# Kernel tuning notes

Measured on AMD Instinct MI355X. Metric: run time of the kernel, lower is better.

## Reference

```python
import jax, jax.numpy as jnp
import numpy as np
import math

B, N, D, H, K = 32, 512, 768, 12, 8  # batch, patches, hidden_dim, heads, n_topic_groups
HD = D // H


def setup_inputs() -> dict:
    key = jax.random.key(0)
    ks = jax.random.split(key, 12)
    hidden_states = jax.random.normal(ks[0], (B, N, D), jnp.float32)
    # group ids in 1..K, every group present (required by original sorted-dict indexing)
    tid = jax.random.permutation(ks[1], (jnp.arange(B, dtype=jnp.int64) % K) + 1)
    s = 1.0 / math.sqrt(D)
    def lin(k):
        kw, kb = jax.random.split(k)
        return (jax.random.normal(kw, (D, D), jnp.float32) * s,
                jax.random.normal(kb, (D,), jnp.float32) * s)
    Wq, bq = lin(ks[2])
    Wk, bk = lin(ks[3])
    Wv, bv = lin(ks[4])
    Wo, bo = lin(ks[5])
    Wc, bc = lin(ks[6])  # Conv1d(D, D, kernel_size=1) == pointwise linear
    return dict(hidden_states=hidden_states, tid=tid, Wq=Wq, bq=bq, Wk=Wk, bk=bk,
                Wv=Wv, bv=bv, Wo=Wo, bo=bo, Wc=Wc, bc=bc)


def reference(hidden_states, tid, Wq, bq, Wk, bk, Wv, bv, Wo, bo, Wc, bc):
    # --- context(): per-group context_aware + mean, scattered back ---
    # context_aware(x) = mean over group of (x + conv1x1(x)); conv is pointwise so
    # it commutes with grouping -> compute per-sample then segment-mean.
    y = hidden_states + jnp.einsum('bnd,ed->bne', hidden_states, Wc) + bc  # [B,N,D]
    seg = tid - 1  # ids are 1..K
    sums = jax.ops.segment_sum(y, seg, num_segments=K)                      # [K,N,D]
    counts = jax.ops.segment_sum(jnp.ones((B,), y.dtype), seg, num_segments=K)
    means = sums / jnp.maximum(counts, 1.0)[:, None, None]
    contexts = means[seg] + hidden_states                                   # [B,N,D]

    # --- dual-stage attention (dropout rate 0 / eval mode) ---
    def heads(x):  # [B,N,D] -> [B,H,N,HD]
        return x.reshape(B, N, H, HD).transpose(0, 2, 1, 3)

    q = heads(hidden_states @ Wq.T + bq)
    t = heads(contexts @ Wq.T + bq)  # topic_states also passes through self.query
    k = heads(hidden_states @ Wk.T + bk)
    v = heads(hidden_states @ Wv.T + bv)

    scale = 1.0 / math.sqrt(HD)
    p1 = jax.nn.softmax(jnp.einsum('bhqd,bhkd->bhqk', t, k) * scale, axis=-1)
    v_t = jnp.einsum('bhqk,bhkd->bhqd', p1, v)
    p2 = jax.nn.softmax(jnp.einsum('bhqd,bhkd->bhqk', q, t) * scale, axis=-1)
    ctx = jnp.einsum('bhqk,bhkd->bhqd', p2, v_t)

    ctx = ctx.transpose(0, 2, 1, 3).reshape(B, N, D)
    return ctx @ Wo.T + bo
```

## Files before the change

kernel.cpp:

```cpp
#include <hip/hip_runtime.h>
#include <hip/hip_bf16.h>


typedef __bf16 bf16_t;
typedef __bf16 bf16x8 __attribute__((ext_vector_type(8)));
typedef __bf16 bf16x4 __attribute__((ext_vector_type(4)));
typedef float f32x4 __attribute__((ext_vector_type(4)));

#define B_ 32
#define N_ 512
#define D_ 768
#define H_ 12
#define HD_ 64
#define K_ 8
#define ND_ (N_ * D_)

typedef __attribute__((address_space(1))) unsigned int as1_u32;
typedef __attribute__((address_space(3))) unsigned int as3_u32;

__device__ __forceinline__ void glds16(const void* g, void* l) {
  __builtin_amdgcn_global_load_lds((as1_u32*)g, (as3_u32*)l, 16, 0, 0);
}

__device__ __forceinline__ f32x4 mfma16(bf16x8 a, bf16x8 b, f32x4 c) {
  return __builtin_amdgcn_mfma_f32_16x16x32_bf16(a, b, c, 0, 0, 0);
}

__device__ __forceinline__ bf16x8 addv8(bf16x8 a, bf16x8 b) {
  bf16x8 o;
#pragma unroll
  for (int j = 0; j < 8; ++j) o[j] = (bf16_t)((float)a[j] + (float)b[j]);
  return o;
}

__device__ __forceinline__ int seg_of(const int* tid, int b) {
  const bool is64 = (tid[1] == 0);
  int v = is64 ? (int)((const long long*)tid)[b] : tid[b];
  return v - 1;
}

__device__ __forceinline__ void gemm_core(const bf16_t* __restrict__ A,
                                          const bf16_t* __restrict__ Bw,
                                          char* smem, f32x4 (&acc)[4][4]) {
  const int t = threadIdx.x;
  const int lane = t & 63, w = t >> 6;
  const int quad = lane >> 4, l15 = lane & 15;
  const int r0 = t >> 2;
  const int c0e = (t & 3) * 8;
  const int wbase = w * 1024;
  const int mRow = (w >> 1) * 64, nCol = (w & 1) * 64;

  const bf16_t* ga0 = A + (size_t)r0 * D_ + c0e;
  const bf16_t* ga1 = A + (size_t)(r0 + 64) * D_ + c0e;
  const bf16_t* gb0 = Bw + (size_t)r0 * D_ + c0e;
  const bf16_t* gb1 = Bw + (size_t)(r0 + 64) * D_ + c0e;

  glds16(ga0, smem + wbase);
  glds16(ga1, smem + 4096 + wbase);
  glds16(gb0, smem + 8192 + wbase);
  glds16(gb1, smem + 12288 + wbase);

  for (int kb = 0; kb < 24; ++kb) {
    __syncthreads();
    char* cur = smem + (kb & 1) * 16384;
    char* nxt = smem + ((kb + 1) & 1) * 16384;
    if (kb < 23) {
      const int ko = (kb + 1) * 32;
      glds16(ga0 + ko, nxt + wbase);
      glds16(ga1 + ko, nxt + 4096 + wbase);
      glds16(gb0 + ko, nxt + 8192 + wbase);
      glds16(gb1 + ko, nxt + 12288 + wbase);
    }
    bf16x8 af[4], bfr[4];
#pragma unroll
    for (int mt = 0; mt < 4; ++mt)
      af[mt] = *(const bf16x8*)(cur + (mRow + mt * 16 + l15) * 64 + quad * 16);
#pragma unroll
    for (int nt = 0; nt < 4; ++nt)
      bfr[nt] = *(const bf16x8*)(cur + 8192 + (nCol + nt * 16 + l15) * 64 +
                                 quad * 16);
#pragma unroll
    for (int mt = 0; mt < 4; ++mt)
#pragma unroll
      for (int nt = 0; nt < 4; ++nt)
        acc[mt][nt] = mfma16(af[mt], bfr[nt], acc[mt][nt]);
  }
}

__device__ __forceinline__ void zero_acc(f32x4 (&acc)[4][4]) {
  const f32x4 z = {0.f, 0.f, 0.f, 0.f};
#pragma unroll
  for (int a = 0; a < 4; ++a)
#pragma unroll
    for (int b = 0; b < 4; ++b) acc[a][b] = z;
}

__global__ __launch_bounds__(256) void k_front(
    const float* __restrict__ x, const float* __restrict__ Wq,
    const float* __restrict__ Wk, const float* __restrict__ Wv,
    const float* __restrict__ Wc, const float* __restrict__ Wo,
    const int* __restrict__ tid, bf16_t* __restrict__ Xb,
    bf16_t* __restrict__ Wqb, bf16_t* __restrict__ Wkb,
    bf16_t* __restrict__ Wvb, bf16_t* __restrict__ Wcb,
    bf16_t* __restrict__ Wob, bf16_t* __restrict__ Mx) {
  if (blockIdx.x < 192) {
    const size_t i = ((size_t)blockIdx.x * 256 + threadIdx.x) * 8;
    float acc[K_][8];
    float cntk[K_];
#pragma unroll
    for (int k = 0; k < K_; ++k) {
      cntk[k] = 0.f;
#pragma unroll
      for (int j = 0; j < 8; ++j) acc[k][j] = 0.f;
    }
    const bool is64 = (tid[1] == 0);
    for (int b = 0; b < B_; ++b) {
      const int s = (is64 ? (int)((const long long*)tid)[b] : tid[b]) - 1;
      const float* p = x + (size_t)b * ND_ + i;
      f32x4 y0 = *(const f32x4*)p;
      f32x4 y1 = *(const f32x4*)(p + 4);
      bf16x8 xo;
#pragma unroll
      for (int j = 0; j < 4; ++j) {
        xo[j] = (bf16_t)y0[j];
        xo[4 + j] = (bf16_t)y1[j];
      }
      *(bf16x8*)(Xb + (size_t)b * ND_ + i) = xo;
#pragma unroll
      for (int k = 0; k < K_; ++k) {
        const float msk = (s == k) ? 1.f : 0.f;
        cntk[k] += msk;
#pragma unroll
        for (int j = 0; j < 4; ++j) {
          acc[k][j] += msk * y0[j];
          acc[k][4 + j] += msk * y1[j];
        }
      }
    }
#pragma unroll
    for (int k = 0; k < K_; ++k) {
      const float inv = 1.f / fmaxf(cntk[k], 1.f);
      bf16x8 o;
#pragma unroll
      for (int j = 0; j < 8; ++j) o[j] = (bf16_t)(acc[k][j] * inv);
      *(bf16x8*)(Mx + (size_t)k * ND_ + i) = o;
    }
    return;
  }
  int bid = blockIdx.x - 192;
  const int wi = bid / 288;
  bid = bid % 288;
  const float* in = wi == 0 ? Wq : wi == 1 ? Wk : wi == 2 ? Wv : wi == 3 ? Wc
                                                                         : Wo;
  bf16_t* out = wi == 0 ? Wqb : wi == 1 ? Wkb : wi == 2 ? Wvb : wi == 3 ? Wcb
                                                                        : Wob;
  const size_t i = ((size_t)bid * 256 + threadIdx.x) * 8;
  f32x4 a = *(const f32x4*)(in + i);
  f32x4 b = *(const f32x4*)(in + i + 4);
  bf16x8 o;
#pragma unroll
  for (int j = 0; j < 4; ++j) { o[j] = (bf16_t)a[j]; o[4 + j] = (bf16_t)b[j]; }
  *(bf16x8*)(out + i) = o;
}

__global__ __launch_bounds__(256, 4) void k_mid(
    const bf16_t* __restrict__ X, const bf16_t* __restrict__ Wq,
    const bf16_t* __restrict__ Wk, const bf16_t* __restrict__ Wv,
    const float* __restrict__ bq, const float* __restrict__ bk,
    const float* __restrict__ bv, bf16_t* __restrict__ Q,
    bf16_t* __restrict__ Kb, bf16_t* __restrict__ V,
    const bf16_t* __restrict__ Mx, const bf16_t* __restrict__ Wcb,
    const float* __restrict__ bc, bf16_t* __restrict__ Mb) {
  __shared__ alignas(16) char smem[32768];
  const int lane = threadIdx.x & 63, w = threadIdx.x >> 6;
  const int quad = lane >> 4, l15 = lane & 15;

  if (blockIdx.x < 192) {
    const int mblk = blockIdx.x / 6, nblk = blockIdx.x % 6;
    f32x4 acc[4][4];
    zero_acc(acc);
    gemm_core(Mx + (size_t)mblk * 128 * D_, Wcb + (size_t)nblk * 128 * D_,
              smem, acc);
    const int mbase = mblk * 128 + (w >> 1) * 64;
    const int nbase = nblk * 128 + (w & 1) * 64;
#pragma unroll
    for (int nt = 0; nt < 4; ++nt) {
      const int col = nbase + nt * 16 + l15;
      const float bb = bc[col];
#pragma unroll
      for (int mt = 0; mt < 4; ++mt)
#pragma unroll
        for (int r = 0; r < 4; ++r) {
          const int row = mbase + mt * 16 + quad * 4 + r;
          const size_t oi = (size_t)row * D_ + col;
          Mb[oi] = (bf16_t)(acc[mt][nt][r] + bb + (float)Mx[oi]);
        }
    }
    return;
  }

  const int qbid = blockIdx.x - 192;
  const int xcd = qbid & 7, i = qbid >> 3;
  const int tile = i % 18, rowblk = (i / 18) * 8 + xcd;
  const int wsel = tile / 6, nb = tile % 6;
  const bf16_t* W = wsel == 0 ? Wq : wsel == 1 ? Wk : Wv;
  const float* bias = wsel == 0 ? bq : wsel == 1 ? bk : bv;
  bf16_t* Out = wsel == 0 ? Q : wsel == 1 ? Kb : V;

  f32x4 acc[4][4];
  zero_acc(acc);
  gemm_core(X + (size_t)rowblk * 128 * D_, W + (size_t)nb * 128 * D_, smem,
            acc);

  const int mbase = rowblk * 128 + (w >> 1) * 64;
  const int nbase = nb * 128 + (w & 1) * 64;
#pragma unroll
  for (int nt = 0; nt < 4; ++nt) {
    const int col = nbase + nt * 16 + l15;
    const float bb = bias[col];
#pragma unroll
    for (int mt = 0; mt < 4; ++mt)
#pragma unroll
      for (int r = 0; r < 4; ++r) {
        const int row = mbase + mt * 16 + quad * 4 + r;
        Out[(size_t)row * D_ + col] = (bf16_t)(acc[mt][nt][r] + bb);
      }
  }
}

__global__ __launch_bounds__(256) void k_gemm_plain(
    const bf16_t* __restrict__ A, const bf16_t* __restrict__ W,
    const float* __restrict__ bias, const bf16_t* __restrict__ addA,
    void* __restrict__ Out, int outF32, int swz) {
  __shared__ alignas(16) char smem[32768];
  int mblk, nblk;
  if (swz) {
    const int bid = blockIdx.x;
    const int xcd = bid & 7, i = bid >> 3;
    nblk = i % 6;
    mblk = (i / 6) * 8 + xcd;
  } else {
    mblk = blockIdx.x;
    nblk = blockIdx.y;
  }
  f32x4 acc[4][4];
  zero_acc(acc);
  gemm_core(A + (size_t)mblk * 128 * D_, W + (size_t)nblk * 128 * D_, smem,
            acc);
  const int lane = threadIdx.x & 63, w = threadIdx.x >> 6;
  const int quad = lane >> 4, l15 = lane & 15;
  const int mbase = mblk * 128 + (w >> 1) * 64;
  const int nbase = nblk * 128 + (w & 1) * 64;
#pragma unroll
  for (int nt = 0; nt < 4; ++nt) {
    const int col = nbase + nt * 16 + l15;
    const float bb = bias ? bias[col] : 0.f;
#pragma unroll
    for (int mt = 0; mt < 4; ++mt)
#pragma unroll
      for (int r = 0; r < 4; ++r) {
        const int row = mbase + mt * 16 + quad * 4 + r;
        float v = acc[mt][nt][r] + bb;
        if (addA) v += (float)addA[(size_t)row * D_ + col];
        const size_t oi = (size_t)row * D_ + col;
        if (outF32) ((float*)Out)[oi] = v;
        else ((bf16_t*)Out)[oi] = (bf16_t)v;
      }
  }
}

__global__ __launch_bounds__(256) void k_attn(const bf16_t* __restrict__ Qp,
                                              const bf16_t* __restrict__ Kp,
                                              const bf16_t* __restrict__ Vp,
                                              const bf16_t* __restrict__ Madd,
                                              const int* __restrict__ tid,
                                              bf16_t* __restrict__ Op,
                                              int addq) {
  __shared__ alignas(16) __bf16 Kt[64][72];
  __shared__ alignas(16) __bf16 Vt[64][72];
  __shared__ alignas(16) __bf16 Pl[4][32][72];

  const int lane = threadIdx.x & 63, w = threadIdx.x >> 6;
  const int quad = lane >> 4, l15 = lane & 15;
  const int b = blockIdx.y / H_, h = blockIdx.y % H_;
  const int q0 = blockIdx.x * 128 + w * 32;
  const size_t base = (size_t)b * ND_ + h * HD_;
  const float C = 0.18033688011112042f;
  const int sg = seg_of(tid, b);
  const bf16_t* Mh = Madd + (size_t)sg * ND_ + h * HD_;

  bf16x8 aq[2][2];
#pragma unroll
  for (int mt = 0; mt < 2; ++mt)
#pragma unroll
    for (int ks = 0; ks < 2; ++ks) {
      const size_t off = (size_t)(q0 + mt * 16 + l15) * D_ + ks * 32 + quad * 8;
      bf16x8 q = *(const bf16x8*)(Qp + base + off);
      if (addq == 1) q = addv8(q, *(const bf16x8*)(Mh + off));
      aq[mt][ks] = q;
    }

  f32x4 O[2][4];
  float lacc[2][4];
  {
    const f32x4 z = {0.f, 0.f, 0.f, 0.f};
#pragma unroll
    for (int mt = 0; mt < 2; ++mt)
#pragma unroll
      for (int nt = 0; nt < 4; ++nt) O[mt][nt] = z;
#pragma unroll
    for (int mt = 0; mt < 2; ++mt)
#pragma unroll
      for (int r = 0; r < 4; ++r) lacc[mt][r] = 0.f;
  }

  const int sr = threadIdx.x >> 2, sc = threadIdx.x & 3;
  const int sig_sr = ((sr & 15) << 2) | (sr >> 4);

  bf16x8 kr[2], vr[2];
#pragma unroll
  for (int half = 0; half < 2; ++half) {
    const int cc = sc + half * 4;
    const size_t off = (size_t)sr * D_ + cc * 8;
    bf16x8 kv = *(const bf16x8*)(Kp + base + off);
    if (addq == 2) kv = addv8(kv, *(const bf16x8*)(Mh + off));
    kr[half] = kv;
    vr[half] = *(const bf16x8*)(Vp + base + off);
  }

  for (int c0 = 0; c0 < N_; c0 += 64) {
    __syncthreads();
#pragma unroll
    for (int half = 0; half < 2; ++half) {
      const int cc = sc + half * 4;
      *(bf16x8*)(&Kt[sr][cc * 8]) = kr[half];
#pragma unroll
      for (int j = 0; j < 8; ++j) Vt[cc * 8 + j][sig_sr] = vr[half][j];
    }
    __syncthreads();

    if (c0 + 64 < N_) {
#pragma unroll
      for (int half = 0; half < 2; ++half) {
        const int cc = sc + half * 4;
        const size_t off = (size_t)(c0 + 64 + sr) * D_ + cc * 8;
        bf16x8 kv = *(const bf16x8*)(Kp + base + off);
        if (addq == 2) kv = addv8(kv, *(const bf16x8*)(Mh + off));
        kr[half] = kv;
        vr[half] = *(const bf16x8*)(Vp + base + off);
      }
    }

    f32x4 S[2][4];
    {
      const f32x4 z = {0.f, 0.f, 0.f, 0.f};
#pragma unroll
      for (int mt = 0; mt < 2; ++mt)
#pragma unroll
        for (int nt = 0; nt < 4; ++nt) S[mt][nt] = z;
    }
#pragma unroll
    for (int ks = 0; ks < 2; ++ks) {
      bf16x8 bk[4];
#pragma unroll
      for (int nt = 0; nt < 4; ++nt)
        bk[nt] = *(const bf16x8*)(&Kt[nt * 16 + l15][ks * 32 + quad * 8]);
#pragma unroll
      for (int mt = 0; mt < 2; ++mt)
#pragma unroll
        for (int nt = 0; nt < 4; ++nt)
          S[mt][nt] = mfma16(aq[mt][ks], bk[nt], S[mt][nt]);
    }

#pragma unroll
    for (int mt = 0; mt < 2; ++mt)
#pragma unroll
      for (int r = 0; r < 4; ++r) {
        bf16x4 pk;
#pragma unroll
        for (int nt = 0; nt < 4; ++nt) {
          const float p = exp2f(S[mt][nt][r] * C);
          lacc[mt][r] += p;
          pk[nt] = (bf16_t)p;
        }
        *(bf16x4*)(&Pl[w][mt * 16 + quad * 4 + r][l15 * 4]) = pk;
      }

#pragma unroll
    for (int ks2 = 0; ks2 < 2; ++ks2) {
      bf16x8 ap[2], bv[4];
#pragma unroll
      for (int mt = 0; mt < 2; ++mt)
        ap[mt] = *(const bf16x8*)(&Pl[w][mt * 16 + l15][ks2 * 32 + quad * 8]);
#pragma unroll
      for (int nt2 = 0; nt2 < 4; ++nt2)
        bv[nt2] = *(const bf16x8*)(&Vt[nt2 * 16 + l15][ks2 * 32 + quad * 8]);
#pragma unroll
      for (int mt = 0; mt < 2; ++mt)
#pragma unroll
        for (int nt2 = 0; nt2 < 4; ++nt2)
          O[mt][nt2] = mfma16(ap[mt], bv[nt2], O[mt][nt2]);
    }
  }

#pragma unroll
  for (int mt = 0; mt < 2; ++mt)
#pragma unroll
    for (int r = 0; r < 4; ++r) {
      float l = lacc[mt][r];
#pragma unroll
      for (int d = 1; d < 16; d <<= 1) l += __shfl_xor(l, d);
      const float inv = 1.f / l;
      const size_t row = base + (size_t)(q0 + mt * 16 + quad * 4 + r) * D_;
#pragma unroll
      for (int nt2 = 0; nt2 < 4; ++nt2)
        Op[row + nt2 * 16 + l15] = (bf16_t)(O[mt][nt2][r] * inv);
    }
}

__global__ __launch_bounds__(256) void k_zero(float* __restrict__ out) {
  const size_t i = ((size_t)blockIdx.x * 256 + threadIdx.x) * 8;
  f32x4 z = {0.f, 0.f, 0.f, 0.f};
  *(f32x4*)(out + i) = z;
  *(f32x4*)(out + i + 4) = z;
}

extern "C" void kernel_launch(void* const* d_in, const int* in_sizes, int n_in,
                              void* d_out, int out_size, void* d_ws,
                              size_t ws_size, hipStream_t stream) {
  const float* x  = (const float*)d_in[0];
  const int*  tid = (const int*)d_in[1];
  const float* Wq = (const float*)d_in[2];
  const float* bq = (const float*)d_in[3];
  const float* Wk = (const float*)d_in[4];
  const float* bk = (const float*)d_in[5];
  const float* Wv = (const float*)d_in[6];
  const float* bv = (const float*)d_in[7];
  const float* Wo = (const float*)d_in[8];
  const float* bo = (const float*)d_in[9];
  const float* Wc = (const float*)d_in[10];
  const float* bc = (const float*)d_in[11];

  const size_t SZ  = (size_t)B_ * ND_ * sizeof(bf16_t);
  const size_t MSZ = (size_t)K_ * ND_ * sizeof(bf16_t);
  const size_t WSZ = (size_t)D_ * D_ * sizeof(bf16_t);
  if (ws_size < 3 * SZ + MSZ + 5 * WSZ) {
    k_zero<<<6144, 256, 0, stream>>>((float*)d_out);
    return;
  }

  char* ws = (char*)d_ws;
  bf16_t* Qb  = (bf16_t*)(ws);
  bf16_t* Kb  = (bf16_t*)(ws + SZ);
  bf16_t* Vb  = (bf16_t*)(ws + 2 * SZ);
  bf16_t* Mq  = (bf16_t*)(ws + 3 * SZ);
  bf16_t* Wqb = (bf16_t*)(ws + 3 * SZ + MSZ);
  bf16_t* Wkb = (bf16_t*)(ws + 3 * SZ + MSZ + WSZ);
  bf16_t* Wvb = (bf16_t*)(ws + 3 * SZ + MSZ + 2 * WSZ);
  bf16_t* Wcb = (bf16_t*)(ws + 3 * SZ + MSZ + 3 * WSZ);
  bf16_t* Wob = (bf16_t*)(ws + 3 * SZ + MSZ + 4 * WSZ);
  bf16_t* Mx  = Mq;
  bf16_t* Mb  = (bf16_t*)d_out;
  bf16_t* VT  = (bf16_t*)d_out;
  bf16_t* Xb  = (bf16_t*)d_out + (size_t)B_ * ND_;
  bf16_t* CTX = Kb;

  k_front<<<1632, 256, 0, stream>>>(x, Wq, Wk, Wv, Wc, Wo, tid, Xb, Wqb, Wkb,
                                    Wvb, Wcb, Wob, Mx);
  k_mid<<<2496, 256, 0, stream>>>(Xb, Wqb, Wkb, Wvb, bq, bk, bv, Qb, Kb, Vb,
                                  Mx, Wcb, bc, Mb);
  k_gemm_plain<<<dim3(32, 6), 256, 0, stream>>>(Mb, Wqb, nullptr, nullptr, Mq,
                                                0, 0);
  k_attn<<<dim3(4, B_ * H_), 256, 0, stream>>>(Qb, Kb, Vb, Mq, tid, VT, 1);
  k_attn<<<dim3(4, B_ * H_), 256, 0, stream>>>(Qb, Qb, VT, Mq, tid, CTX, 2);
  k_gemm_plain<<<768, 256, 0, stream>>>(CTX, Wob, bo, nullptr, d_out, 1, 1);
}
```

Baseline: 397.2 us.

## Fold conv1x1 weight into query projection to drop a GEMM pass

Precomputes a combined weight Wq·(I+Wc) and bias Wq·bc in the front kernel, so the group-mean topic queries come from one GEMM on the group means instead of a conv GEMM followed by a separate query GEMM. This removes one kernel launch and the intermediate Mb round trip. In exchange the front kernel gains a small fp32-input weight GEMM and a bias matvec, and the rounding changes because the folded weight is stored in bf16.

```diff
diff --git a/kernel.cpp b/kernel.cpp
--- a/kernel.cpp
+++ b/kernel.cpp
@@ -99,12 +99,108 @@
     const float* __restrict__ x, const float* __restrict__ Wq,
     const float* __restrict__ Wk, const float* __restrict__ Wv,
     const float* __restrict__ Wc, const float* __restrict__ Wo,
-    const int* __restrict__ tid, bf16_t* __restrict__ Xb,
-    bf16_t* __restrict__ Wqb, bf16_t* __restrict__ Wkb,
-    bf16_t* __restrict__ Wvb, bf16_t* __restrict__ Wcb,
-    bf16_t* __restrict__ Wob, bf16_t* __restrict__ Mx) {
-  if (blockIdx.x < 192) {
-    const size_t i = ((size_t)blockIdx.x * 256 + threadIdx.x) * 8;
+    const float* __restrict__ bc, const int* __restrict__ tid,
+    bf16_t* __restrict__ Xb, bf16_t* __restrict__ Wqb,
+    bf16_t* __restrict__ Wkb, bf16_t* __restrict__ Wvb,
+    bf16_t* __restrict__ Wcb, bf16_t* __restrict__ Wob,
+    bf16_t* __restrict__ Mx, bf16_t* __restrict__ Wqcb,
+    float* __restrict__ bq2) {
+  __shared__ alignas(16) char smem[16384];
+  const int t = threadIdx.x;
+
+  if (blockIdx.x < 36) {
+    const int mblk = blockIdx.x / 6, nblk = blockIdx.x % 6;
+    const int lane = t & 63, w = t >> 6;
+    const int quad = lane >> 4, l15 = lane & 15;
+    const int mRow = (w >> 1) * 64, nCol = (w & 1) * 64;
+    const int ar = t >> 2, ac = (t & 3) * 8;
+    const int bd = t >> 3, bc0 = (t & 7) * 16;
+    const float* gA0 = Wq + (size_t)(mblk * 128 + ar) * D_ + ac;
+    const float* gA1 = gA0 + (size_t)64 * D_;
+    const float* gB = Wc + (size_t)bd * D_ + nblk * 128 + bc0;
+
+    f32x4 a0[2], a1[2], bv[4];
+    auto loadt = [&](int kb) {
+      const int ko = kb * 32;
+      a0[0] = *(const f32x4*)(gA0 + ko);
+      a0[1] = *(const f32x4*)(gA0 + ko + 4);
+      a1[0] = *(const f32x4*)(gA1 + ko);
+      a1[1] = *(const f32x4*)(gA1 + ko + 4);
+      const float* pb = gB + (size_t)ko * D_;
+#pragma unroll
+      for (int j = 0; j < 4; ++j) bv[j] = *(const f32x4*)(pb + j * 4);
+    };
+    f32x4 acc[4][4];
+    zero_acc(acc);
+    loadt(0);
+    for (int kb = 0; kb < 24; ++kb) {
+      __syncthreads();
+      {
+        bf16x8 av0, av1;
+#pragma unroll
+        for (int j = 0; j < 4; ++j) {
+          av0[j] = (bf16_t)a0[0][j]; av0[4 + j] = (bf16_t)a0[1][j];
+          av1[j] = (bf16_t)a1[0][j]; av1[4 + j] = (bf16_t)a1[1][j];
+        }
+        *(bf16x8*)(smem + ar * 64 + (t & 3) * 16) = av0;
+        *(bf16x8*)(smem + 4096 + ar * 64 + (t & 3) * 16) = av1;
+        bf16_t* bl = (bf16_t*)(smem + 8192);
+#pragma unroll
+        for (int j = 0; j < 4; ++j)
+#pragma unroll
+          for (int jj = 0; jj < 4; ++jj)
+            bl[(bc0 + j * 4 + jj) * 32 + bd] = (bf16_t)bv[j][jj];
+      }
+      __syncthreads();
+      if (kb < 23) loadt(kb + 1);
+      bf16x8 af[4], bfr[4];
+#pragma unroll
+      for (int mt = 0; mt < 4; ++mt)
+        af[mt] = *(const bf16x8*)(smem + (mRow + mt * 16 + l15) * 64 +
+                                  quad * 16);
+#pragma unroll
+      for (int nt = 0; nt < 4; ++nt)
+        bfr[nt] = *(const bf16x8*)(smem + 8192 + (nCol + nt * 16 + l15) * 64 +
+                                   quad * 16);
+#pragma unroll
+      for (int mt = 0; mt < 4; ++mt)
+#pragma unroll
+        for (int nt = 0; nt < 4; ++nt)
+          acc[mt][nt] = mfma16(af[mt], bfr[nt], acc[mt][nt]);
+    }
+    const int mbase = mblk * 128 + mRow;
+    const int nbase = nblk * 128 + nCol;
+#pragma unroll
+    for (int nt = 0; nt < 4; ++nt) {
+      const int col = nbase + nt * 16 + l15;
+#pragma unroll
+      for (int mt = 0; mt < 4; ++mt)
+#pragma unroll
+        for (int r = 0; r < 4; ++r) {
+          const int row = mbase + mt * 16 + quad * 4 + r;
+          const size_t oi = (size_t)row * D_ + col;
+          Wqcb[oi] = (bf16_t)(acc[mt][nt][r] + Wq[oi]);
+        }
+    }
+    return;
+  }
+
+  if (blockIdx.x < 39) {
+    const int e = (blockIdx.x - 36) * 256 + t;
+    const float* wr = Wq + (size_t)e * D_;
+    float s = 0.f;
+    for (int d = 0; d < D_; d += 4) {
+      f32x4 wv = *(const f32x4*)(wr + d);
+      f32x4 bv = *(const f32x4*)(bc + d);
+#pragma unroll
+      for (int j = 0; j < 4; ++j) s += wv[j] * bv[j];
+    }
+    bq2[e] = s;
+    return;
+  }
+
+  if (blockIdx.x < 231) {
+    const size_t i = ((size_t)(blockIdx.x - 39) * 256 + t) * 8;
     float acc[K_][8];
     float cntk[K_];
 #pragma unroll
@@ -147,14 +243,14 @@
     }
     return;
   }
-  int bid = blockIdx.x - 192;
+  int bid = blockIdx.x - 231;
   const int wi = bid / 288;
   bid = bid % 288;
   const float* in = wi == 0 ? Wq : wi == 1 ? Wk : wi == 2 ? Wv : wi == 3 ? Wc
                                                                          : Wo;
   bf16_t* out = wi == 0 ? Wqb : wi == 1 ? Wkb : wi == 2 ? Wvb : wi == 3 ? Wcb
                                                                         : Wob;
-  const size_t i = ((size_t)bid * 256 + threadIdx.x) * 8;
+  const size_t i = ((size_t)bid * 256 + t) * 8;
   f32x4 a = *(const f32x4*)(in + i);
   f32x4 b = *(const f32x4*)(in + i + 4);
   bf16x8 o;
@@ -169,8 +265,8 @@
     const float* __restrict__ bq, const float* __restrict__ bk,
     const float* __restrict__ bv, bf16_t* __restrict__ Q,
     bf16_t* __restrict__ Kb, bf16_t* __restrict__ V,
-    const bf16_t* __restrict__ Mx, const bf16_t* __restrict__ Wcb,
-    const float* __restrict__ bc, bf16_t* __restrict__ Mb) {
+    const bf16_t* __restrict__ Mx, const bf16_t* __restrict__ Wqcb,
+    const float* __restrict__ bq2, bf16_t* __restrict__ Mq) {
   __shared__ alignas(16) char smem[32768];
   const int lane = threadIdx.x & 63, w = threadIdx.x >> 6;
   const int quad = lane >> 4, l15 = lane & 15;
@@ -179,21 +275,20 @@
     const int mblk = blockIdx.x / 6, nblk = blockIdx.x % 6;
     f32x4 acc[4][4];
     zero_acc(acc);
-    gemm_core(Mx + (size_t)mblk * 128 * D_, Wcb + (size_t)nblk * 128 * D_,
+    gemm_core(Mx + (size_t)mblk * 128 * D_, Wqcb + (size_t)nblk * 128 * D_,
               smem, acc);
     const int mbase = mblk * 128 + (w >> 1) * 64;
     const int nbase = nblk * 128 + (w & 1) * 64;
 #pragma unroll
     for (int nt = 0; nt < 4; ++nt) {
       const int col = nbase + nt * 16 + l15;
-      const float bb = bc[col];
+      const float bb = bq2[col];
 #pragma unroll
       for (int mt = 0; mt < 4; ++mt)
 #pragma unroll
         for (int r = 0; r < 4; ++r) {
           const int row = mbase + mt * 16 + quad * 4 + r;
-          const size_t oi = (size_t)row * D_ + col;
-          Mb[oi] = (bf16_t)(acc[mt][nt][r] + bb + (float)Mx[oi]);
+          Mq[(size_t)row * D_ + col] = (bf16_t)(acc[mt][nt][r] + bb);
         }
     }
     return;
@@ -459,18 +554,17 @@
   bf16_t* Wvb = (bf16_t*)(ws + 3 * SZ + MSZ + 2 * WSZ);
   bf16_t* Wcb = (bf16_t*)(ws + 3 * SZ + MSZ + 3 * WSZ);
   bf16_t* Wob = (bf16_t*)(ws + 3 * SZ + MSZ + 4 * WSZ);
-  bf16_t* Mx  = Mq;
-  bf16_t* Mb  = (bf16_t*)d_out;
-  bf16_t* VT  = (bf16_t*)d_out;
-  bf16_t* Xb  = (bf16_t*)d_out + (size_t)B_ * ND_;
-  bf16_t* CTX = Kb;
-
-  k_front<<<1632, 256, 0, stream>>>(x, Wq, Wk, Wv, Wc, Wo, tid, Xb, Wqb, Wkb,
-                                    Wvb, Wcb, Wob, Mx);
+  bf16_t* Wqcb = (bf16_t*)d_out;
+  float*  bq2  = (float*)((char*)d_out + 2 * 1024 * 1024);
+  bf16_t* Mx   = (bf16_t*)((char*)d_out + 8 * 1024 * 1024);
+  bf16_t* VT   = (bf16_t*)d_out;
+  bf16_t* Xb   = (bf16_t*)d_out + (size_t)B_ * ND_;
+  bf16_t* CTX  = Kb;
+
+  k_front<<<1671, 256, 0, stream>>>(x, Wq, Wk, Wv, Wc, Wo, bc, tid, Xb, Wqb,
+                                    Wkb, Wvb, Wcb, Wob, Mx, Wqcb, bq2);
   k_mid<<<2496, 256, 0, stream>>>(Xb, Wqb, Wkb, Wvb, bq, bk, bv, Qb, Kb, Vb,
-                                  Mx, Wcb, bc, Mb);
-  k_gemm_plain<<<dim3(32, 6), 256, 0, stream>>>(Mb, Wqb, nullptr, nullptr, Mq,
-                                                0, 0);
+                                  Mx, Wqcb, bq2, Mq);
   k_attn<<<dim3(4, B_ * H_), 256, 0, stream>>>(Qb, Kb, Vb, Mq, tid, VT, 1);
   k_attn<<<dim3(4, B_ * H_), 256, 0, stream>>>(Qb, Qb, VT, Mq, tid, CTX, 2);
   k_gemm_plain<<<768, 256, 0, stream>>>(CTX, Wob, bo, nullptr, d_out, 1, 1);
```

Result: no change. 398.0 us (+0.2%).
